# Kernel tuning notes

Measured on AMD Instinct MI355X. Metric: run time of the kernel, lower is better.

Reference implementation:

```python
import jax, jax.numpy as jnp
import numpy as np

C = 512
CQ = C // 8
BN_EPS = 1e-5


def setup_inputs() -> dict:
    key = jax.random.key(0)
    ks = jax.random.split(key, 12)
    s = 0.02
    return {
        "x": jax.random.normal(ks[0], (4, C, 64, 64), dtype=jnp.float32),
        "qw": jax.random.normal(ks[1], (CQ, C), dtype=jnp.float32) * s,
        "qb": jnp.zeros((CQ,), dtype=jnp.float32),
        "kw": jax.random.normal(ks[2], (CQ, C), dtype=jnp.float32) * s,
        "kb": jnp.zeros((CQ,), dtype=jnp.float32),
        "vw": jax.random.normal(ks[3], (C, C), dtype=jnp.float32) * s,
        "vb": jnp.zeros((C,), dtype=jnp.float32),
        "gamma": jnp.zeros((1,), dtype=jnp.float32),
        "beta": jnp.zeros((1,), dtype=jnp.float32),
        "fw": jax.random.normal(ks[4], (C, 2 * C), dtype=jnp.float32) * s,
        "fb": jnp.zeros((C,), dtype=jnp.float32),
        "bn_w": jnp.ones((C,), dtype=jnp.float32),
        "bn_b": jnp.zeros((C,), dtype=jnp.float32),
    }


def reference(x, qw, qb, kw, kb, vw, vb, gamma, beta, fw, fb, bn_w, bn_b):
    b, c, h, w = x.shape
    n = h * w
    xf = x.reshape(b, c, n)  # [b, c, n]

    # ----- position attention -----
    q = jnp.einsum('oc,bcn->bon', qw, xf) + qb[None, :, None]  # [b, cq, n]
    k = jnp.einsum('oc,bcn->bon', kw, xf) + kb[None, :, None]
    v = jnp.einsum('oc,bcn->bon', vw, xf) + vb[None, :, None]  # [b, c, n]
    # scores[i, j] = q_i . k_j, softmax over j
    scores = jnp.einsum('bci,bcj->bij', q, k)  # [b, n, n]
    att = jax.nn.softmax(scores, axis=-1)
    pos = jnp.einsum('bcj,bij->bci', v, att)  # [b, c, n]
    pos_out = (gamma[0] * pos + xf).reshape(b, c, h, w)

    # ----- channel attention -----
    energy = jnp.einsum('bin,bjn->bij', xf, xf)  # [b, c, c]
    catt = jax.nn.softmax(energy, axis=-1)
    chan = jnp.einsum('bij,bjn->bin', catt, xf)
    chan_out = (beta[0] * chan + xf).reshape(b, c, h, w)

    # ----- fusion: 1x1 conv + BN (batch stats, training mode) + ReLU -----
    cat = jnp.concatenate([pos_out, chan_out], axis=1)  # [b, 2c, h, w]
    y = jnp.einsum('oc,bchw->bohw', fw, cat) + fb[None, :, None, None]
    mean = jnp.mean(y, axis=(0, 2, 3), keepdims=True)
    var = jnp.var(y, axis=(0, 2, 3), keepdims=True)
    yn = (y - mean) * jax.lax.rsqrt(var + BN_EPS)
    out = jax.nn.relu(yn * bn_w[None, :, None, None] + bn_b[None, :, None, None])
    return out
```

## Files before the change

kernel.cpp:

```cpp
#include <hip/hip_runtime.h>
#include <stdint.h>

typedef unsigned short u16;
typedef __attribute__((ext_vector_type(8))) short bf16x8;
typedef __attribute__((ext_vector_type(4))) float f32x4;

#define DEVI static __device__ __forceinline__

DEVI u16 f2bf(float f){
  union { float f; uint32_t u; } c; c.f = f;
  uint32_t u = c.u;
  u += 0x7FFFu + ((u >> 16) & 1u);
  return (u16)(u >> 16);
}
DEVI float b2f(u16 h){
  union { uint32_t u; float f; } c; c.u = ((uint32_t)h) << 16;
  return c.f;
}

DEVI void gload16(const u16* g, u16* l){
  __builtin_amdgcn_global_load_lds(
      (const __attribute__((address_space(1))) unsigned int*)g,
      (__attribute__((address_space(3))) unsigned int*)l, 16, 0, 0);
}

DEVI bf16x8 ldsrd(const void* base, int byte){
  return *reinterpret_cast<const bf16x8*>((const char*)base + byte);
}

template<int BM,int BN,int FM,int FN,int BIAS,int EPI,int SWZ,int KSPLIT=1>
__global__ __launch_bounds__(256) void gemm_bt(
    const u16* __restrict__ A, long long strideA, int lda,
    const u16* __restrict__ B, long long strideB, int ldb,
    void* __restrict__ C, long long strideC, int ldc,
    const float* __restrict__ bias, int K,
    const float* __restrict__ cscale, const u16* __restrict__ xadd,
    long long strideX, int ldx)
{
  constexpr int BK  = 32;
  constexpr int WTM = FM*16, WTN = FN*16;
  static_assert(BM == 2*WTM && BN == 2*WTN, "2x2 wave layout");
  __shared__ u16 As[BM*BK];
  __shared__ u16 Bs[BN*BK];

  int bx = blockIdx.x, by = blockIdx.y, bz = blockIdx.z;
  if(SWZ){
    const int gx = gridDim.x, gy = gridDim.y;
    const int nwg = gx * gy * gridDim.z;
    const int orig = bx + gx * (by + gy * bz);
    const int q = nwg >> 3, r = nwg & 7;
    const int xcd = orig & 7, i = orig >> 3;
    const int wg = (xcd < r ? xcd*(q+1) : r*(q+1) + (xcd-r)*q) + i;
    bx = wg % gx;
    const int t = wg / gx;
    by = t % gy;
    bz = t / gy;
  }

  const int zz = bz;
  const int z  = (KSPLIT > 1) ? zz / KSPLIT : zz;
  const int ks = (KSPLIT > 1) ? zz % KSPLIT : 0;
  const u16* Ab = A + (long long)z * strideA + (long long)ks * K;
  const u16* Bb = B + (long long)z * strideB + (long long)ks * K;

  const int tid  = threadIdx.x;
  const int lane = tid & 63, wid = tid >> 6;
  const int wr = wid >> 1, wc = wid & 1;
  const long long bm0 = (long long)by * BM;
  const long long bn0 = (long long)bx * BN;

  const int srow  = lane >> 2;
  const int scol  = (((lane & 3) ^ ((lane >> 3) & 3))) * 8;
  const int wrow  = wid * 16 + srow;
  constexpr int TA = BM/64, TB = BN/64;

  const int fr  = lane & 15;
  const int sl8 = ((lane >> 4) ^ ((lane >> 1) & 3)) * 8;

  f32x4 acc[FM][FN] = {};

  for(int k0 = 0; k0 < K; k0 += BK){
    __syncthreads();
    #pragma unroll
    for(int t=0;t<TA;t++)
      gload16(&Ab[(bm0 + t*64 + wrow)*lda + k0 + scol],
              &As[(t*64 + wid*16)*BK]);
    #pragma unroll
    for(int t=0;t<TB;t++)
      gload16(&Bb[(bn0 + t*64 + wrow)*ldb + k0 + scol],
              &Bs[(t*64 + wid*16)*BK]);
    __syncthreads();

    bf16x8 af[FM], bg[FN];
    #pragma unroll
    for(int m=0;m<FM;m++)
      af[m] = *reinterpret_cast<const bf16x8*>(&As[(wr*WTM + m*16 + fr)*BK + sl8]);
    #pragma unroll
    for(int n=0;n<FN;n++)
      bg[n] = *reinterpret_cast<const bf16x8*>(&Bs[(wc*WTN + n*16 + fr)*BK + sl8]);
    #pragma unroll
    for(int m=0;m<FM;m++)
      #pragma unroll
      for(int n=0;n<FN;n++)
        acc[m][n] = __builtin_amdgcn_mfma_f32_16x16x32_bf16(af[m], bg[n], acc[m][n], 0, 0, 0);
  }

  const int lr = (lane >> 4) * 4, lc = lane & 15;
  const float g = (EPI == 3) ? cscale[0] : 0.f;
  #pragma unroll
  for(int m=0;m<FM;m++){
    #pragma unroll
    for(int n=0;n<FN;n++){
      #pragma unroll
      for(int r=0;r<4;r++){
        long long row = bm0 + wr*WTM + m*16 + lr + r;
        long long col = bn0 + wc*WTN + n*16 + lc;
        float v = acc[m][n][r];
        if(BIAS == 1) v += bias[(int)row];
        if(BIAS == 2) v += bias[(int)col];
        long long idx = row * (long long)ldc + col;
        if(EPI == 0){
          ((float*)C + (long long)zz*strideC)[idx] = v;
        } else if(EPI == 1){
          ((float*)C + (long long)zz*strideC)[idx] += v;
        } else if(EPI == 2){
          ((u16*)C + (long long)zz*strideC)[idx] = f2bf(v);
        } else {
          float xv = b2f(xadd[(long long)z*strideX + row*(long long)ldx + col]);
          ((u16*)C + (long long)zz*strideC)[idx] = f2bf(g * v + xv);
        }
      }
    }
  }
}

__global__ __launch_bounds__(512, 4) void flash_pos(
    const u16* __restrict__ qkT,
    const u16* __restrict__ vB,
    const u16* __restrict__ xfT,
    u16* __restrict__ pcT,
    const float* __restrict__ gamma)
{
  __shared__ u16 Ks[2][64*64];
  __shared__ u16 Vs[256*64];
  __shared__ u16 Ps[64*64];
  __shared__ float RS[2][4][32];

  int flat = blockIdx.x + 64*(blockIdx.y + 2*blockIdx.z);
  flat = (flat & 7)*64 + (flat >> 3);
  const int bx = flat & 63;
  const int ch = (flat >> 6) & 1;
  const int z  = flat >> 7;

  const int q0 = bx*64, c0 = ch*256;
  const int tid = threadIdx.x, lane = tid & 63, wid = tid >> 6;
  const int wr = wid >> 2, wc = wid & 3;
  const int fr = lane & 15, fq = lane >> 4;

  const u16* qkb = qkT + (long long)z*4096*128;
  const u16* vbb = vB  + (long long)z*512*4096;

  const int srow  = lane >> 3;
  const int sslot = (lane & 7) ^ srow;

  bf16x8 qa[2][2];
  #pragma unroll
  for(int m=0;m<2;m++)
    #pragma unroll
    for(int kk=0;kk<2;kk++)
      qa[m][kk] = *reinterpret_cast<const bf16x8*>(
          &qkb[(long long)(q0 + wr*32 + m*16 + fr)*128 + kk*32 + fq*8]);

  const u16* kp = qkb + (long long)(wid*8 + srow)*128 + 64 + sslot*8;
  const u16* vp0 = vbb + (long long)(c0 +   0 + wid*8 + srow)*4096 + sslot*8;
  const u16* vp1 = vbb + (long long)(c0 +  64 + wid*8 + srow)*4096 + sslot*8;
  const u16* vp2 = vbb + (long long)(c0 + 128 + wid*8 + srow)*4096 + sslot*8;
  const u16* vp3 = vbb + (long long)(c0 + 192 + wid*8 + srow)*4096 + sslot*8;

  const int xm   = (fr & 7) << 4;
  const int koff = (wc*16 + fr)*128 + ((fq*16) ^ xm);
  const int pab  = (wr*32 + fr)*128 + ((fq*16) ^ xm);
  const int vbb0 = (wc*64 + fr)*128 + ((fq*16) ^ xm);
  const int kdst = wid * 1024;
  const int key2 = (wc*16 + fr)*2;
  int pwo[4];
  #pragma unroll
  for(int r=0;r<4;r++){
    int qr = fq*4 + r;
    pwo[r] = qr*128 + (key2 ^ ((qr & 7) << 4));
  }

  gload16(kp, (u16*)((char*)Ks + kdst));
  kp += 64*128;
  gload16(vp0, &Vs[(  0 + wid*8)*64]);
  gload16(vp1, &Vs[( 64 + wid*8)*64]);
  gload16(vp2, &Vs[(128 + wid*8)*64]);
  gload16(vp3, &Vs[(192 + wid*8)*64]);
  vp0 += 64; vp1 += 64; vp2 += 64; vp3 += 64;
  __syncthreads();

  f32x4 acc[2][4] = {};
  float rsacc[2][4] = {};

  for(int t=0;t<64;t++){
    const int kbase = (t & 1) ? 8192 : 0;
    bf16x8 kb0 = ldsrd(Ks, kbase + koff);
    bf16x8 kb1 = ldsrd(Ks, kbase + (koff ^ 64));
    f32x4 s[2] = {};
    #pragma unroll
    for(int m=0;m<2;m++){
      s[m] = __builtin_amdgcn_mfma_f32_16x16x32_bf16(qa[m][0], kb0, s[m], 0, 0, 0);
      s[m] = __builtin_amdgcn_mfma_f32_16x16x32_bf16(qa[m][1], kb1, s[m], 0, 0, 0);
    }

    #pragma unroll
    for(int m=0;m<2;m++){
      #pragma unroll
      for(int r=0;r<4;r++){
        float e = __expf(s[m][r]);
        rsacc[m][r] += e;
        *(u16*)((char*)Ps + (pwo[r] + wr*4096 + m*2048)) = f2bf(e);
      }
    }
    __syncthreads();

    if(t+1 < 64){
      gload16(kp, (u16*)((char*)Ks + (kbase ^ 8192) + kdst));
      kp += 64*128;
    }

    bf16x8 pa00 = ldsrd(Ps, pab);
    bf16x8 pa01 = ldsrd(Ps, pab ^ 64);
    bf16x8 pa10 = ldsrd(Ps, (pab + 2048));
    bf16x8 pa11 = ldsrd(Ps, (pab + 2048) ^ 64);
    __builtin_amdgcn_s_setprio(1);
    #pragma unroll
    for(int n=0;n<4;n++){
      bf16x8 v0 = ldsrd(Vs, vbb0 + n*2048);
      bf16x8 v1 = ldsrd(Vs, (vbb0 + n*2048) ^ 64);
      acc[0][n] = __builtin_amdgcn_mfma_f32_16x16x32_bf16(pa00, v0, acc[0][n], 0, 0, 0);
      acc[0][n] = __builtin_amdgcn_mfma_f32_16x16x32_bf16(pa01, v1, acc[0][n], 0, 0, 0);
      acc[1][n] = __builtin_amdgcn_mfma_f32_16x16x32_bf16(pa10, v0, acc[1][n], 0, 0, 0);
      acc[1][n] = __builtin_amdgcn_mfma_f32_16x16x32_bf16(pa11, v1, acc[1][n], 0, 0, 0);
    }
    __builtin_amdgcn_s_setprio(0);
    __syncthreads();

    if(t+1 < 64){
      gload16(vp0, &Vs[(  0 + wid*8)*64]);
      gload16(vp1, &Vs[( 64 + wid*8)*64]);
      gload16(vp2, &Vs[(128 + wid*8)*64]);
      gload16(vp3, &Vs[(192 + wid*8)*64]);
      vp0 += 64; vp1 += 64; vp2 += 64; vp3 += 64;
    }
  }

  #pragma unroll
  for(int m=0;m<2;m++)
    #pragma unroll
    for(int r=0;r<4;r++){
      float v = rsacc[m][r];
      #pragma unroll
      for(int o=1;o<16;o<<=1) v += __shfl_xor(v, o);
      rsacc[m][r] = v;
    }
  if(fr == 0){
    #pragma unroll
    for(int m=0;m<2;m++)
      #pragma unroll
      for(int r=0;r<4;r++)
        RS[wr][wc][m*16 + fq*4 + r] = rsacc[m][r];
  }
  __syncthreads();

  const float g = gamma[0];
  #pragma unroll
  for(int m=0;m<2;m++){
    float inv[4];
    #pragma unroll
    for(int r=0;r<4;r++){
      int rloc = m*16 + fq*4 + r;
      inv[r] = g / (RS[wr][0][rloc] + RS[wr][1][rloc] +
                    RS[wr][2][rloc] + RS[wr][3][rloc]);
    }
    #pragma unroll
    for(int n=0;n<4;n++){
      #pragma unroll
      for(int r=0;r<4;r++){
        int qrow = q0 + wr*32 + m*16 + fq*4 + r;
        int c    = c0 + wc*64 + n*16 + fr;
        float xv = b2f(xfT[((long long)z*4096 + qrow)*512 + c]);
        pcT[((long long)z*4096 + qrow)*1024 + c] = f2bf(acc[m][n][r]*inv[r] + xv);
      }
    }
  }
}

__global__ __launch_bounds__(256) void softmax_sum4(const float* __restrict__ part,
                                                    u16* __restrict__ catt)
{
  const int row = blockIdx.x;
  const int b = row >> 9, i = row & 511;
  const int t = threadIdx.x;
  const int lane = t & 63, wid = t >> 6;
  float v[2];
  #pragma unroll
  for(int j=0;j<2;j++){
    int col = j*256 + t;
    float s = 0.f;
    #pragma unroll
    for(int sl=0;sl<4;sl++)
      s += part[(((long long)(b*4 + sl)*512 + i)*512) + col];
    v[j] = s;
  }
  float m = fmaxf(v[0], v[1]);
  #pragma unroll
  for(int o=32;o;o>>=1) m = fmaxf(m, __shfl_xor(m, o));
  __shared__ float sred[4];
  if(lane == 0) sred[wid] = m;
  __syncthreads();
  m = fmaxf(fmaxf(sred[0], sred[1]), fmaxf(sred[2], sred[3]));
  float e0 = __expf(v[0] - m), e1 = __expf(v[1] - m);
  float s = e0 + e1;
  #pragma unroll
  for(int o=32;o;o>>=1) s += __shfl_xor(s, o);
  __syncthreads();
  if(lane == 0) sred[wid] = s;
  __syncthreads();
  s = sred[0] + sred[1] + sred[2] + sred[3];
  float inv = 1.0f / s;
  u16* op = catt + (long long)row * 512;
  op[t]       = f2bf(e0 * inv);
  op[256 + t] = f2bf(e1 * inv);
}

__global__ __launch_bounds__(256) void prep_weights(
    const float* __restrict__ qw, const float* __restrict__ kw,
    const float* __restrict__ vw, const float* __restrict__ fw,
    const float* __restrict__ qb, const float* __restrict__ kb,
    u16* __restrict__ qkwb, u16* __restrict__ vwb, u16* __restrict__ fwb,
    float* __restrict__ qkb)
{
  long long i = (long long)blockIdx.x*256 + threadIdx.x;
  const float* src; u16* dst; long long o;
  if(i < 8192){        src = qw; dst = qkwb;          o = i; }
  else if(i < 16384){  src = kw; dst = qkwb + 32768;  o = i - 8192; }
  else if(i < 81920){  src = vw; dst = vwb;           o = i - 16384; }
  else if(i < 212992){ src = fw; dst = fwb;           o = i - 81920; }
  else if(i < 213024){
    int t = (int)(i - 212992) * 4;
    #pragma unroll
    for(int j=0;j<4;j++) qkb[t+j] = (t+j < 64) ? qb[t+j] : kb[t+j-64];
    return;
  } else return;
  float4 v = reinterpret_cast<const float4*>(src)[o];
  ushort4 w;
  w.x = f2bf(v.x); w.y = f2bf(v.y); w.z = f2bf(v.z); w.w = f2bf(v.w);
  reinterpret_cast<ushort4*>(dst)[o] = w;
}

__global__ __launch_bounds__(256) void transpose_cast(
    const float* __restrict__ x, u16* __restrict__ xfb, u16* __restrict__ xfT)
{
  __shared__ float tile[32][33];
  const int b  = blockIdx.z;
  const int n0 = blockIdx.x * 32, c0 = blockIdx.y * 32;
  const int tx = threadIdx.x, ty = threadIdx.y;
  const float* xp = x + (long long)b * 512 * 4096;
  #pragma unroll
  for(int i=0;i<4;i++){
    int c = c0 + ty + i*8;
    float v = xp[(long long)c*4096 + n0 + tx];
    tile[ty + i*8][tx] = v;
    xfb[((long long)b*512 + c)*4096 + n0 + tx] = f2bf(v);
  }
  __syncthreads();
  #pragma unroll
  for(int i=0;i<4;i++){
    int n = n0 + ty + i*8;
    xfT[((long long)b*4096 + n)*512 + c0 + tx] = f2bf(tile[tx][ty + i*8]);
  }
}

__global__ __launch_bounds__(256) void bn_stats(const float* __restrict__ y,
                                                float* __restrict__ stat)
{
  const int o = blockIdx.x, t = threadIdx.x;
  const int lane = t & 63, wid = t >> 6;
  float s = 0.f, ss = 0.f;
  for(int b=0;b<4;b++){
    const float* p = y + ((long long)b*512 + o)*4096;
    for(int i=t;i<4096;i+=256){ float v = p[i]; s += v; ss += v*v; }
  }
  #pragma unroll
  for(int off=32;off;off>>=1){ s += __shfl_xor(s, off); ss += __shfl_xor(ss, off); }
  __shared__ float sred[8];
  if(lane == 0){ sred[wid] = s; sred[wid+4] = ss; }
  __syncthreads();
  if(t == 0){
    float S  = sred[0]+sred[1]+sred[2]+sred[3];
    float SS = sred[4]+sred[5]+sred[6]+sred[7];
    float mean = S * (1.f/16384.f);
    float var  = SS * (1.f/16384.f) - mean*mean;
    stat[o*2]   = mean;
    stat[o*2+1] = rsqrtf(var + 1e-5f);
  }
}

__global__ __launch_bounds__(256) void bn_apply(float* __restrict__ y,
    const float* __restrict__ stat, const float* __restrict__ w,
    const float* __restrict__ bb)
{
  long long i = (long long)blockIdx.x*256 + threadIdx.x;
  float4 v = reinterpret_cast<float4*>(y)[i];
  int o = (int)(((i*4) >> 12) & 511);
  float mean = stat[o*2], rstd = stat[o*2+1];
  float sc = w[o] * rstd;
  float sh = bb[o] - mean * sc;
  v.x = fmaxf(v.x*sc + sh, 0.f);
  v.y = fmaxf(v.y*sc + sh, 0.f);
  v.z = fmaxf(v.z*sc + sh, 0.f);
  v.w = fmaxf(v.w*sc + sh, 0.f);
  reinterpret_cast<float4*>(y)[i] = v;
}

extern "C" void kernel_launch(void* const* d_in, const int* in_sizes, int n_in,
                              void* d_out, int out_size, void* d_ws, size_t ws_size,
                              hipStream_t stream)
{
  const float* x     = (const float*)d_in[0];
  const float* qw    = (const float*)d_in[1];
  const float* qb    = (const float*)d_in[2];
  const float* kw    = (const float*)d_in[3];
  const float* kb    = (const float*)d_in[4];
  const float* vw    = (const float*)d_in[5];
  const float* vb    = (const float*)d_in[6];
  const float* gamma = (const float*)d_in[7];
  const float* beta  = (const float*)d_in[8];
  const float* fw    = (const float*)d_in[9];
  const float* fb    = (const float*)d_in[10];
  const float* bnw   = (const float*)d_in[11];
  const float* bnb   = (const float*)d_in[12];
  float* out = (float*)d_out;
  (void)in_sizes; (void)n_in; (void)out_size; (void)ws_size;

  char* base = (char*)d_ws;
  size_t off = 0;
  auto alloc = [&](size_t bytes)->char* {
    char* p = base + off;
    off += (bytes + 255) & ~(size_t)255;
    return p;
  };
  const long long NB = 4, Cc = 512, Nn = 4096;

  u16*   xfT  = (u16*)alloc((size_t)NB*Nn*Cc*2);
  u16*   xfb  = (u16*)alloc((size_t)NB*Cc*Nn*2);
  u16*   qkwb = (u16*)alloc((size_t)128*Cc*2);
  float* qkb  = (float*)alloc(128*4);
  u16*   vwb  = (u16*)alloc((size_t)Cc*Cc*2);
  u16*   fwb  = (u16*)alloc((size_t)Cc*2*Cc*2);
  u16*   qkT  = (u16*)alloc((size_t)NB*Nn*128*2);
  u16*   vB   = (u16*)alloc((size_t)NB*Cc*Nn*2);
  u16*   pcT  = (u16*)alloc((size_t)NB*Nn*1024*2);
  float* epart= (float*)alloc((size_t)16*Cc*Cc*4);
  u16*   catt = (u16*)alloc((size_t)NB*Cc*Cc*2);
  float* stat = (float*)alloc((size_t)Cc*2*4);

  prep_weights<<<dim3(833), dim3(256), 0, stream>>>(qw, kw, vw, fw, qb, kb,
                                                    qkwb, vwb, fwb, qkb);
  transpose_cast<<<dim3(128,16,4), dim3(32,8), 0, stream>>>(x, xfb, xfT);

  gemm_bt<64,64,2,2,2,2,1><<<dim3(2,64,4), dim3(256), 0, stream>>>(
      xfT, Nn*Cc, 512, qkwb, 0, 512, qkT, Nn*128, 128, qkb, 512,
      nullptr, nullptr, 0, 0);
  gemm_bt<128,128,4,4,1,2,1><<<dim3(32,4,4), dim3(256), 0, stream>>>(
      vwb, 0, 512, xfT, Nn*Cc, 512, vB, Cc*Nn, 4096, vb, 512,
      nullptr, nullptr, 0, 0);

  gemm_bt<128,128,4,4,0,0,1,4><<<dim3(4,4,16), dim3(256), 0, stream>>>(
      xfb, Cc*Nn, 4096, xfb, Cc*Nn, 4096, epart, Cc*Cc, 512, nullptr, 1024,
      nullptr, nullptr, 0, 0);
  softmax_sum4<<<dim3(2048), dim3(256), 0, stream>>>(epart, catt);
  gemm_bt<128,128,4,4,0,3,1><<<dim3(4,32,4), dim3(256), 0, stream>>>(
      xfT, Nn*Cc, 512, catt, Cc*Cc, 512, pcT + 512, Nn*1024, 1024, nullptr, 512,
      beta, xfT, Nn*Cc, 512);

  flash_pos<<<dim3(64,2,4), dim3(512), 0, stream>>>(qkT, vB, xfT, pcT, gamma);

  gemm_bt<128,128,4,4,1,0,1><<<dim3(32,4,4), dim3(256), 0, stream>>>(
      fwb, 0, 1024, pcT, Nn*1024, 1024, out, Cc*Nn, 4096, fb, 1024,
      nullptr, nullptr, 0, 0);

  bn_stats<<<dim3(512), dim3(256), 0, stream>>>(out, stat);
  bn_apply<<<dim3(8192), dim3(256), 0, stream>>>(out, stat, bnw, bnb);
}
```

Before: 258.5 us.

## Split flash P·V over keys, use exp2 with prescaled Q, store energy partials in bf16

flash_pos now has its two wave rows split the key dimension of the P·V product, each covering all 64 query rows. This halves per-wave V LDS reads and needs a shared-memory reduction of accumulators at the end. The exponent uses exp2f with log2e folded into the Q weights and bias, and bf16 packing uses a packed convert instruction. Channel-energy partials are stored as bf16 rather than fp32, cutting traffic at some precision cost, and softmax_sum4 uses packed 32-bit loads and stores.

```diff
diff --git a/kernel.cpp b/kernel.cpp
--- a/kernel.cpp
+++ b/kernel.cpp
@@ -141,9 +141,11 @@
     u16* __restrict__ pcT,
     const float* __restrict__ gamma)
 {
-  __shared__ u16 Ks[2][64*64];
-  __shared__ u16 Vs[256*64];
-  __shared__ u16 Ps[64*64];
+  __shared__ char SMEM[57344];
+  u16* Ks = (u16*)SMEM;
+  u16* Vs = (u16*)(SMEM + 16384);
+  u16* Ps = (u16*)(SMEM + 49152);
+  float* arena = (float*)SMEM;
   __shared__ float RS[2][4][32];
 
   int flat = blockIdx.x + 64*(blockIdx.y + 2*blockIdx.z);
@@ -171,16 +173,14 @@
       qa[m][kk] = *reinterpret_cast<const bf16x8*>(
           &qkb[(long long)(q0 + wr*32 + m*16 + fr)*128 + kk*32 + fq*8]);
 
-  const u16* kp = qkb + (long long)(wid*8 + srow)*128 + 64 + sslot*8;
-  const u16* vp0 = vbb + (long long)(c0 +   0 + wid*8 + srow)*4096 + sslot*8;
-  const u16* vp1 = vbb + (long long)(c0 +  64 + wid*8 + srow)*4096 + sslot*8;
-  const u16* vp2 = vbb + (long long)(c0 + 128 + wid*8 + srow)*4096 + sslot*8;
-  const u16* vp3 = vbb + (long long)(c0 + 192 + wid*8 + srow)*4096 + sslot*8;
+  const u16* kp  = qkb + (long long)(wid*8 + srow)*128 + 64 + sslot*8;
+  const u16* vp0 = vbb + (long long)(c0 + wid*8 + srow)*4096 + sslot*8;
 
   const int xm   = (fr & 7) << 4;
   const int koff = (wc*16 + fr)*128 + ((fq*16) ^ xm);
-  const int pab  = (wr*32 + fr)*128 + ((fq*16) ^ xm);
-  const int vbb0 = (wc*64 + fr)*128 + ((fq*16) ^ xm);
+  const int pvx  = (wr*64 + fq*16) ^ xm;
+  const int pab  = fr*128 + pvx;
+  const int vfb  = (wc*64 + fr)*128 + pvx;
   const int kdst = wid * 1024;
   const int key2 = (wc*16 + fr)*2;
   int pwo[4];
@@ -192,14 +192,14 @@
 
   gload16(kp, (u16*)((char*)Ks + kdst));
   kp += 64*128;
-  gload16(vp0, &Vs[(  0 + wid*8)*64]);
-  gload16(vp1, &Vs[( 64 + wid*8)*64]);
-  gload16(vp2, &Vs[(128 + wid*8)*64]);
-  gload16(vp3, &Vs[(192 + wid*8)*64]);
-  vp0 += 64; vp1 += 64; vp2 += 64; vp3 += 64;
-  __syncthreads();
-
-  f32x4 acc[2][4] = {};
+  gload16(vp0,            &Vs[(  0 + wid*8)*64]);
+  gload16(vp0 +  64*4096, &Vs[( 64 + wid*8)*64]);
+  gload16(vp0 + 128*4096, &Vs[(128 + wid*8)*64]);
+  gload16(vp0 + 192*4096, &Vs[(192 + wid*8)*64]);
+  vp0 += 64;
+  __syncthreads();
+
+  f32x4 acc[4][4] = {};
   float rsacc[2][4] = {};
 
   for(int t=0;t<64;t++){
@@ -215,12 +215,18 @@
 
     #pragma unroll
     for(int m=0;m<2;m++){
-      #pragma unroll
-      for(int r=0;r<4;r++){
-        float e = __expf(s[m][r]);
-        rsacc[m][r] += e;
-        *(u16*)((char*)Ps + (pwo[r] + wr*4096 + m*2048)) = f2bf(e);
-      }
+      float e0 = exp2f(s[m][0]), e1 = exp2f(s[m][1]);
+      float e2 = exp2f(s[m][2]), e3 = exp2f(s[m][3]);
+      rsacc[m][0] += e0; rsacc[m][1] += e1;
+      rsacc[m][2] += e2; rsacc[m][3] += e3;
+      uint32_t p01, p23;
+      asm("v_cvt_pk_bf16_f32 %0, %1, %2" : "=v"(p01) : "v"(e0), "v"(e1));
+      asm("v_cvt_pk_bf16_f32 %0, %1, %2" : "=v"(p23) : "v"(e2), "v"(e3));
+      char* pbase = (char*)Ps + wr*4096 + m*2048;
+      *(u16*)(pbase + pwo[0]) = (u16)p01;
+      *(u16*)(pbase + pwo[1]) = (u16)(p01 >> 16);
+      *(u16*)(pbase + pwo[2]) = (u16)p23;
+      *(u16*)(pbase + pwo[3]) = (u16)(p23 >> 16);
     }
     __syncthreads();
 
@@ -229,29 +235,28 @@
       kp += 64*128;
     }
 
-    bf16x8 pa00 = ldsrd(Ps, pab);
-    bf16x8 pa01 = ldsrd(Ps, pab ^ 64);
-    bf16x8 pa10 = ldsrd(Ps, (pab + 2048));
-    bf16x8 pa11 = ldsrd(Ps, (pab + 2048) ^ 64);
+    bf16x8 pa0 = ldsrd(Ps, pab);
+    bf16x8 pa1 = ldsrd(Ps, pab + 2048);
+    bf16x8 pa2 = ldsrd(Ps, pab + 4096);
+    bf16x8 pa3 = ldsrd(Ps, pab + 6144);
     __builtin_amdgcn_s_setprio(1);
     #pragma unroll
     for(int n=0;n<4;n++){
-      bf16x8 v0 = ldsrd(Vs, vbb0 + n*2048);
-      bf16x8 v1 = ldsrd(Vs, (vbb0 + n*2048) ^ 64);
-      acc[0][n] = __builtin_amdgcn_mfma_f32_16x16x32_bf16(pa00, v0, acc[0][n], 0, 0, 0);
-      acc[0][n] = __builtin_amdgcn_mfma_f32_16x16x32_bf16(pa01, v1, acc[0][n], 0, 0, 0);
-      acc[1][n] = __builtin_amdgcn_mfma_f32_16x16x32_bf16(pa10, v0, acc[1][n], 0, 0, 0);
-      acc[1][n] = __builtin_amdgcn_mfma_f32_16x16x32_bf16(pa11, v1, acc[1][n], 0, 0, 0);
+      bf16x8 v = ldsrd(Vs, vfb + n*2048);
+      acc[0][n] = __builtin_amdgcn_mfma_f32_16x16x32_bf16(pa0, v, acc[0][n], 0, 0, 0);
+      acc[1][n] = __builtin_amdgcn_mfma_f32_16x16x32_bf16(pa1, v, acc[1][n], 0, 0, 0);
+      acc[2][n] = __builtin_amdgcn_mfma_f32_16x16x32_bf16(pa2, v, acc[2][n], 0, 0, 0);
+      acc[3][n] = __builtin_amdgcn_mfma_f32_16x16x32_bf16(pa3, v, acc[3][n], 0, 0, 0);
     }
     __builtin_amdgcn_s_setprio(0);
     __syncthreads();
 
     if(t+1 < 64){
-      gload16(vp0, &Vs[(  0 + wid*8)*64]);
-      gload16(vp1, &Vs[( 64 + wid*8)*64]);
-      gload16(vp2, &Vs[(128 + wid*8)*64]);
-      gload16(vp3, &Vs[(192 + wid*8)*64]);
-      vp0 += 64; vp1 += 64; vp2 += 64; vp3 += 64;
+      gload16(vp0,            &Vs[(  0 + wid*8)*64]);
+      gload16(vp0 +  64*4096, &Vs[( 64 + wid*8)*64]);
+      gload16(vp0 + 128*4096, &Vs[(128 + wid*8)*64]);
+      gload16(vp0 + 192*4096, &Vs[(192 + wid*8)*64]);
+      vp0 += 64;
     }
   }
 
@@ -271,56 +276,97 @@
       for(int r=0;r<4;r++)
         RS[wr][wc][m*16 + fq*4 + r] = rsacc[m][r];
   }
-  __syncthreads();
-
-  const float g = gamma[0];
-  #pragma unroll
-  for(int m=0;m<2;m++){
-    float inv[4];
-    #pragma unroll
-    for(int r=0;r<4;r++){
-      int rloc = m*16 + fq*4 + r;
-      inv[r] = g / (RS[wr][0][rloc] + RS[wr][1][rloc] +
-                    RS[wr][2][rloc] + RS[wr][3][rloc]);
-    }
-    #pragma unroll
-    for(int n=0;n<4;n++){
+
+  const int aslot = (wc & 1) * 4096;
+  if(wr == 1 && wc < 2){
+    #pragma unroll
+    for(int m=0;m<4;m++)
+      #pragma unroll
+      for(int n=0;n<4;n++)
+        #pragma unroll
+        for(int r=0;r<4;r++)
+          arena[aslot + (m*16 + fq*4 + r)*64 + n*16 + fr] = acc[m][n][r];
+  }
+  __syncthreads();
+  if(wr == 0 && wc < 2){
+    #pragma unroll
+    for(int m=0;m<4;m++)
+      #pragma unroll
+      for(int n=0;n<4;n++)
+        #pragma unroll
+        for(int r=0;r<4;r++)
+          acc[m][n][r] += arena[aslot + (m*16 + fq*4 + r)*64 + n*16 + fr];
+  }
+  __syncthreads();
+  if(wr == 1 && wc >= 2){
+    #pragma unroll
+    for(int m=0;m<4;m++)
+      #pragma unroll
+      for(int n=0;n<4;n++)
+        #pragma unroll
+        for(int r=0;r<4;r++)
+          arena[aslot + (m*16 + fq*4 + r)*64 + n*16 + fr] = acc[m][n][r];
+  }
+  __syncthreads();
+  if(wr == 0 && wc >= 2){
+    #pragma unroll
+    for(int m=0;m<4;m++)
+      #pragma unroll
+      for(int n=0;n<4;n++)
+        #pragma unroll
+        for(int r=0;r<4;r++)
+          acc[m][n][r] += arena[aslot + (m*16 + fq*4 + r)*64 + n*16 + fr];
+  }
+
+  if(wr == 0){
+    const float g = gamma[0];
+    #pragma unroll
+    for(int m=0;m<4;m++){
+      float inv[4];
       #pragma unroll
       for(int r=0;r<4;r++){
-        int qrow = q0 + wr*32 + m*16 + fq*4 + r;
-        int c    = c0 + wc*64 + n*16 + fr;
-        float xv = b2f(xfT[((long long)z*4096 + qrow)*512 + c]);
-        pcT[((long long)z*4096 + qrow)*1024 + c] = f2bf(acc[m][n][r]*inv[r] + xv);
+        int q = m*16 + fq*4 + r;
+        int wrq = q >> 5, rloc = q & 31;
+        inv[r] = g / (RS[wrq][0][rloc] + RS[wrq][1][rloc] +
+                      RS[wrq][2][rloc] + RS[wrq][3][rloc]);
       }
-    }
-  }
-}
-
-__global__ __launch_bounds__(256) void softmax_sum4(const float* __restrict__ part,
+      #pragma unroll
+      for(int n=0;n<4;n++){
+        #pragma unroll
+        for(int r=0;r<4;r++){
+          int qrow = q0 + m*16 + fq*4 + r;
+          int c    = c0 + wc*64 + n*16 + fr;
+          float xv = b2f(xfT[((long long)z*4096 + qrow)*512 + c]);
+          pcT[((long long)z*4096 + qrow)*1024 + c] = f2bf(acc[m][n][r]*inv[r] + xv);
+        }
+      }
+    }
+  }
+}
+
+__global__ __launch_bounds__(256) void softmax_sum4(const u16* __restrict__ part,
                                                     u16* __restrict__ catt)
 {
   const int row = blockIdx.x;
   const int b = row >> 9, i = row & 511;
   const int t = threadIdx.x;
   const int lane = t & 63, wid = t >> 6;
-  float v[2];
-  #pragma unroll
-  for(int j=0;j<2;j++){
-    int col = j*256 + t;
-    float s = 0.f;
-    #pragma unroll
-    for(int sl=0;sl<4;sl++)
-      s += part[(((long long)(b*4 + sl)*512 + i)*512) + col];
-    v[j] = s;
-  }
-  float m = fmaxf(v[0], v[1]);
+  float v0 = 0.f, v1 = 0.f;
+  #pragma unroll
+  for(int sl=0;sl<4;sl++){
+    uint32_t pr = *reinterpret_cast<const uint32_t*>(
+        &part[(((long long)(b*4 + sl)*512 + i)*512) + 2*t]);
+    v0 += b2f((u16)pr);
+    v1 += b2f((u16)(pr >> 16));
+  }
+  float m = fmaxf(v0, v1);
   #pragma unroll
   for(int o=32;o;o>>=1) m = fmaxf(m, __shfl_xor(m, o));
   __shared__ float sred[4];
   if(lane == 0) sred[wid] = m;
   __syncthreads();
   m = fmaxf(fmaxf(sred[0], sred[1]), fmaxf(sred[2], sred[3]));
-  float e0 = __expf(v[0] - m), e1 = __expf(v[1] - m);
+  float e0 = __expf(v0 - m), e1 = __expf(v1 - m);
   float s = e0 + e1;
   #pragma unroll
   for(int o=32;o;o>>=1) s += __shfl_xor(s, o);
@@ -329,9 +375,8 @@
   __syncthreads();
   s = sred[0] + sred[1] + sred[2] + sred[3];
   float inv = 1.0f / s;
-  u16* op = catt + (long long)row * 512;
-  op[t]       = f2bf(e0 * inv);
-  op[256 + t] = f2bf(e1 * inv);
+  uint32_t pk = (uint32_t)f2bf(e0 * inv) | ((uint32_t)f2bf(e1 * inv) << 16);
+  *reinterpret_cast<uint32_t*>(&catt[(long long)row * 512 + 2*t]) = pk;
 }
 
 __global__ __launch_bounds__(256) void prep_weights(
@@ -341,21 +386,22 @@
     u16* __restrict__ qkwb, u16* __restrict__ vwb, u16* __restrict__ fwb,
     float* __restrict__ qkb)
 {
+  const float LOG2E = 1.4426950408889634f;
   long long i = (long long)blockIdx.x*256 + threadIdx.x;
-  const float* src; u16* dst; long long o;
-  if(i < 8192){        src = qw; dst = qkwb;          o = i; }
+  const float* src; u16* dst; long long o; float sc = 1.f;
+  if(i < 8192){        src = qw; dst = qkwb;          o = i; sc = LOG2E; }
   else if(i < 16384){  src = kw; dst = qkwb + 32768;  o = i - 8192; }
   else if(i < 81920){  src = vw; dst = vwb;           o = i - 16384; }
   else if(i < 212992){ src = fw; dst = fwb;           o = i - 81920; }
   else if(i < 213024){
     int t = (int)(i - 212992) * 4;
     #pragma unroll
-    for(int j=0;j<4;j++) qkb[t+j] = (t+j < 64) ? qb[t+j] : kb[t+j-64];
+    for(int j=0;j<4;j++) qkb[t+j] = (t+j < 64) ? qb[t+j]*LOG2E : kb[t+j-64];
     return;
   } else return;
   float4 v = reinterpret_cast<const float4*>(src)[o];
   ushort4 w;
-  w.x = f2bf(v.x); w.y = f2bf(v.y); w.z = f2bf(v.z); w.w = f2bf(v.w);
+  w.x = f2bf(v.x*sc); w.y = f2bf(v.y*sc); w.z = f2bf(v.z*sc); w.w = f2bf(v.w*sc);
   reinterpret_cast<ushort4*>(dst)[o] = w;
 }
 
@@ -462,7 +508,7 @@
   u16*   qkT  = (u16*)alloc((size_t)NB*Nn*128*2);
   u16*   vB   = (u16*)alloc((size_t)NB*Cc*Nn*2);
   u16*   pcT  = (u16*)alloc((size_t)NB*Nn*1024*2);
-  float* epart= (float*)alloc((size_t)16*Cc*Cc*4);
+  u16*   epart= (u16*)alloc((size_t)16*Cc*Cc*2);
   u16*   catt = (u16*)alloc((size_t)NB*Cc*Cc*2);
   float* stat = (float*)alloc((size_t)Cc*2*4);
 
@@ -477,7 +523,7 @@
       vwb, 0, 512, xfT, Nn*Cc, 512, vB, Cc*Nn, 4096, vb, 512,
       nullptr, nullptr, 0, 0);
 
-  gemm_bt<128,128,4,4,0,0,1,4><<<dim3(4,4,16), dim3(256), 0, stream>>>(
+  gemm_bt<128,128,4,4,0,2,1,4><<<dim3(4,4,16), dim3(256), 0, stream>>>(
       xfb, Cc*Nn, 4096, xfb, Cc*Nn, 4096, epart, Cc*Cc, 512, nullptr, 1024,
       nullptr, nullptr, 0, 0);
   softmax_sum4<<<dim3(2048), dim3(256), 0, stream>>>(epart, catt);
```

New measurement: 300.4 us. 16.2% more time.
